# Kernel tuning notes

Measured on AMD Instinct MI355X. Metric: run time of the kernel, lower is better.

The kernel has to match this reference:

```python
import jax, jax.numpy as jnp
import numpy as np

MAX_WAVELENGTH = 1000.0

def _sine_pos(n, d):
    # keras_nlp SinePositionEncoding with max_wavelength=1000
    pos = jnp.arange(n, dtype=jnp.float32)
    i = jnp.arange(d)
    timescales = (1.0 / MAX_WAVELENGTH) ** ((2 * (i // 2)).astype(jnp.float32) / d)
    ang = pos[:, None] * timescales[None, :]  # (n, d)
    return jnp.where(i % 2 == 0, jnp.sin(ang), jnp.cos(ang))


def setup_inputs() -> dict:
    key = jax.random.key(0)
    ks = jax.random.split(key, 6)
    B, N, D, H, O = 4, 2048, 512, 8, 64
    inputs = jax.random.normal(ks[0], (B, N, D), jnp.float32)
    mem = jax.random.normal(ks[1], (B, H, O, O), jnp.float32) * 0.02
    # z accumulates sums of (elu(k)+1) > 0, so keep it positive
    z = jax.random.uniform(ks[2], (B, H, O), jnp.float32) + 1.0
    attn_kernel = jax.random.normal(ks[3], (D, H, O, 3), jnp.float32) * (1.0 / np.sqrt(D))
    out_kernel = jax.random.normal(ks[4], (O, H, O), jnp.float32) * (1.0 / np.sqrt(O * H))
    beta = jnp.zeros((1,), jnp.float32)
    return dict(inputs=inputs, mem=mem, z=z, attn_kernel=attn_kernel,
                out_kernel=out_kernel, beta=beta)


def reference(inputs, mem, z, attn_kernel, out_kernel, beta):
    B, N, D = inputs.shape
    x = inputs + _sine_pos(N, D)[None].astype(inputs.dtype)
    # fused QKV projection: (B,N,H,dims,3)
    kvq = jnp.einsum('bni,ihok->bnhok', x, attn_kernel)
    k, v, q = kvq[..., 0], kvq[..., 1], kvq[..., 2]
    # linear-attention memory readout
    q_elu = jax.nn.elu(q) + 1.0
    num = jnp.einsum('bhdo,bnhd->bnho', mem, q_elu)
    den = jnp.einsum('bhd,bnhd->bnh', z, q_elu)[..., None] + 1e-8
    A_mem = num / den
    # delta-rule state update
    k_elu = jax.nn.elu(k) + 1.0
    next_mem = mem + jnp.einsum('bnhz,bnho->bhzo', k_elu, v - A_mem)
    next_z = z + k_elu.sum(axis=1)
    # causal softmax attention over the chunk
    scale = jnp.sqrt(jnp.asarray(D, inputs.dtype))
    qk = jnp.einsum('bnho,bkho->bhnk', q, k) / scale
    mask = -(1.0 - jnp.tril(jnp.ones((N, N), inputs.dtype))) * 1e10
    A_soft = jax.nn.softmax(qk + mask, axis=-1)
    A_dot = jnp.einsum('bhnk,bkho->bnho', A_soft, v)
    # sigmoid-gated mix + output projection
    g = jax.nn.sigmoid(beta)  # (1,) broadcasts
    A = g * A_mem + (1.0 - g) * A_dot
    out = jnp.einsum('bnhi,iho->bno', A, out_kernel)
    return out, next_mem, next_z
```

## Files before the change

### kernel.cpp

```cpp
#include <hip/hip_runtime.h>
#include <hip/hip_bf16.h>
#include <math.h>

#define BB 4
#define SEQ 2048
#define DIM 512
#define NH 8
#define HD 64

typedef __attribute__((ext_vector_type(8))) short short8;
typedef __attribute__((ext_vector_type(4))) float f32x4;

static __device__ inline ushort f2bf(float f) {
    __hip_bfloat16 h = __float2bfloat16(f);
    union { __hip_bfloat16 h; ushort u; } cv;
    cv.h = h;
    return cv.u;
}
static __device__ inline float bf2f(ushort u) {
    return __uint_as_float((uint)u << 16);
}

#define GLOAD16(g, l)                                                          \
    __builtin_amdgcn_global_load_lds(                                          \
        (const __attribute__((address_space(1))) uint32_t*)(g),                \
        (__attribute__((address_space(3))) uint32_t*)(l), 16, 0, 0)

__global__ __launch_bounds__(256) void pos_add_bf16_kernel(const float* __restrict__ in,
                                                           ushort* __restrict__ xbf) {
    int idx = blockIdx.x * 256 + threadIdx.x;
    int p = idx & 255;
    int n = (idx >> 8) & 2047;
    float e = (float)(2 * p) * (1.0f / 512.0f);
    float ts = __expf(-6.907755278982137f * e);
    float arev = (float)n * (ts * 0.15915494309189535f);
    float f = arev - floorf(arev);
    float s = __builtin_amdgcn_sinf(f);
    float c = __builtin_amdgcn_cosf(f);
    float2 v = *(const float2*)(in + (size_t)idx * 2);
    uint pack = (uint)f2bf(v.x + s) | ((uint)f2bf(v.y + c) << 16);
    ((uint*)xbf)[idx] = pack;
}

__global__ __launch_bounds__(256) void wconv_kernel(const float* __restrict__ w,
                                                    ushort* __restrict__ wt) {
    __shared__ float tile[64][129];
    int ib = blockIdx.x;
    int jb = blockIdx.y;
    int t = threadIdx.x;
    #pragma unroll
    for (int u = 0; u < 8; ++u) {
        int idx = u * 1024 + t * 4;
        int r = idx >> 7, j = idx & 127;
        float4 v = *(const float4*)(w + (size_t)(ib * 64 + r) * 1536 + jb * 128 + j);
        tile[r][j] = v.x; tile[r][j + 1] = v.y; tile[r][j + 2] = v.z; tile[r][j + 3] = v.w;
    }
    __syncthreads();
    int j = t >> 1;
    int rh = (t & 1) * 32;
    int jg = jb * 128 + j;
    int h = jg / 192;
    int rem = jg - h * 192;
    int o = rem / 3;
    int c = rem - o * 3;
    int nrow = c * 512 + h * 64 + o;
    #pragma unroll
    for (int s8 = 0; s8 < 4; ++s8) {
        short8 pk;
        #pragma unroll
        for (int q = 0; q < 8; ++q) pk[q] = (short)f2bf(tile[rh + s8 * 8 + q][j]);
        *(short8*)(wt + (size_t)nrow * 512 + ib * 64 + rh + s8 * 8) = pk;
    }
}

__global__ __launch_bounds__(256) void wout_conv_kernel(const float* __restrict__ wo,
                                                        ushort* __restrict__ wobf) {
    int g = blockIdx.x * 256 + threadIdx.x;
    int o2 = g >> 9, k = g & 511;
    int h = k >> 6, i = k & 63;
    wobf[g] = f2bf(wo[(size_t)i * 512 + h * 64 + o2]);
}

__global__ __launch_bounds__(256) void qkv_mfma_kernel(const ushort* __restrict__ xbf,
                                                       const ushort* __restrict__ wt,
                                                       ushort* __restrict__ kbf,
                                                       ushort* __restrict__ vbf,
                                                       ushort* __restrict__ qbf) {
    __shared__ __align__(16) ushort As[128 * 32];
    __shared__ __align__(16) ushort Bs[128 * 32];
    int t = threadIdx.x;
    int w = t >> 6, lane = t & 63, l15 = lane & 15, lg = lane >> 4;
    int wr = w >> 1, wc = w & 1;
    int m0 = blockIdx.x * 128;
    int by = blockIdx.y;
    int n0 = by * 128;
    f32x4 acc[4][4] = {};
    int srow = t >> 2, scol = (t & 3) * 8;
    const ushort* ag = xbf + (size_t)(m0 + srow) * 512 + scol;
    const ushort* bg = wt + (size_t)(n0 + srow) * 512 + scol;
    ushort* as_dst = As + t * 8;
    ushort* bs_dst = Bs + t * 8;

    for (int k0 = 0; k0 < 512; k0 += 32) {
        __syncthreads();
        GLOAD16(ag + k0, as_dst);
        GLOAD16(ag + k0 + 64 * 512, as_dst + 64 * 32);
        GLOAD16(bg + k0, bs_dst);
        GLOAD16(bg + k0 + 64 * 512, bs_dst + 64 * 32);
        __syncthreads();
        short8 af[4], bf[4];
        #pragma unroll
        for (int mi = 0; mi < 4; ++mi)
            af[mi] = *(const short8*)&As[(wr * 64 + mi * 16 + l15) * 32 + lg * 8];
        #pragma unroll
        for (int ni = 0; ni < 4; ++ni)
            bf[ni] = *(const short8*)&Bs[(wc * 64 + ni * 16 + l15) * 32 + lg * 8];
        #pragma unroll
        for (int mi = 0; mi < 4; ++mi)
            #pragma unroll
            for (int ni = 0; ni < 4; ++ni)
                acc[mi][ni] = __builtin_amdgcn_mfma_f32_16x16x32_bf16(af[mi], bf[ni], acc[mi][ni], 0, 0, 0);
    }

    ushort* dst = (by < 4) ? kbf : (by < 8) ? vbf : qbf;
    int ho0 = (by & 3) * 128 + wc * 64;
    int mb = m0 + wr * 64;
    #pragma unroll
    for (int mi = 0; mi < 4; ++mi)
        #pragma unroll
        for (int ni = 0; ni < 4; ++ni)
            #pragma unroll
            for (int r = 0; r < 4; ++r)
                dst[(size_t)(mb + mi * 16 + lg * 4 + r) * 512 + ho0 + ni * 16 + l15] =
                    f2bf(acc[mi][ni][r]);
}

__global__ __launch_bounds__(256) void vt_kernel(const ushort* __restrict__ vbf,
                                                 ushort* __restrict__ vtbf) {
    int bid = blockIdx.x;
    int nt = bid & 31;
    int bh = bid >> 5;
    int b = bh >> 3, h = bh & 7;
    __shared__ ushort tile[64][72];
    int t = threadIdx.x;
    {
        int n = t >> 2, dc = (t & 3) * 16;
        const ushort* src = vbf + (size_t)(b * 2048 + nt * 64 + n) * 512 + h * 64 + dc;
        *(short8*)&tile[n][dc] = *(const short8*)src;
        *(short8*)&tile[n][dc + 8] = *(const short8*)(src + 8);
    }
    __syncthreads();
    {
        int d = t >> 2, nc = (t & 3) * 16;
        ushort* dst = vtbf + (size_t)bh * 64 * 2048 + (size_t)d * 2048 + nt * 64 + nc;
        short8 a, bq;
        #pragma unroll
        for (int j = 0; j < 8; ++j) { a[j] = (short)tile[nc + j][d]; bq[j] = (short)tile[nc + 8 + j][d]; }
        *(short8*)dst = a;
        *(short8*)(dst + 8) = bq;
    }
}

__global__ __launch_bounds__(256) void amem_kernel(const ushort* __restrict__ qbf,
                                                   const float* __restrict__ mem,
                                                   const float* __restrict__ zin,
                                                   ushort* __restrict__ ambf) {
    int bid = blockIdx.x;
    int ntile = bid & 7;
    int h = (bid >> 3) & 7;
    int b = bid >> 6;
    __shared__ __align__(16) float mem_s[4096];
    __shared__ float z_s[64];
    int t = threadIdx.x;
    const float* msrc = mem + (size_t)(b * 8 + h) * 4096;
    #pragma unroll
    for (int u = 0; u < 16; ++u) mem_s[t + 256 * u] = msrc[t + 256 * u];
    if (t < 64) z_s[t] = zin[(b * 8 + h) * 64 + t];
    __syncthreads();
    int n = ntile * 256 + t;
    const ushort* qrow = qbf + (size_t)(b * 2048 + n) * 512 + h * 64;
    float qe[64];
    #pragma unroll
    for (int d8 = 0; d8 < 8; ++d8) {
        short8 v8 = *(const short8*)(qrow + d8 * 8);
        #pragma unroll
        for (int j = 0; j < 8; ++j) {
            float f = bf2f((ushort)v8[j]);
            qe[d8 * 8 + j] = f > 0.f ? f + 1.f : __expf(f);
        }
    }
    float den = 0.f;
    #pragma unroll
    for (int d = 0; d < 64; ++d) den += z_s[d] * qe[d];
    den += 1e-8f;
    float num[64];
    #pragma unroll
    for (int o = 0; o < 64; ++o) num[o] = 0.f;
    #pragma unroll
    for (int d = 0; d < 64; ++d) {
        float qd = qe[d];
        #pragma unroll
        for (int o4 = 0; o4 < 64; o4 += 4) {
            float4 mv = *(const float4*)&mem_s[d * 64 + o4];
            num[o4 + 0] += mv.x * qd;
            num[o4 + 1] += mv.y * qd;
            num[o4 + 2] += mv.z * qd;
            num[o4 + 3] += mv.w * qd;
        }
    }
    float inv = 1.f / den;
    ushort* dst = ambf + (size_t)(b * 2048 + n) * 512 + h * 64;
    #pragma unroll
    for (int o8 = 0; o8 < 8; ++o8) {
        short8 pk;
        #pragma unroll
        for (int j = 0; j < 8; ++j) pk[j] = (short)f2bf(num[o8 * 8 + j] * inv);
        *(short8*)(dst + o8 * 8) = pk;
    }
}

__global__ __launch_bounds__(256) void delta_part_kernel(const ushort* __restrict__ kbf,
                                                         const ushort* __restrict__ vbf,
                                                         const ushort* __restrict__ ambf,
                                                         float* __restrict__ part,
                                                         float* __restrict__ zpart) {
    int bid = blockIdx.x;
    int bh = bid & 31;
    int chunk = bid >> 5;
    int h = bh & 7, b = bh >> 3;
    __shared__ __align__(16) float ke_s[2048];
    __shared__ __align__(16) float vm_s[2048];
    int t = threadIdx.x;
    int tx = t & 15, ty = t >> 4;
    float acc[4][4] = {};
    float nz = 0.f;
    int nbase = chunk * 256;
    for (int n0 = 0; n0 < 256; n0 += 32) {
        {
            int nn = t >> 3, cc = (t & 7) * 8;
            size_t g = (size_t)(b * 2048 + nbase + n0 + nn) * 512 + h * 64 + cc;
            short8 k8 = *(const short8*)(kbf + g);
            short8 v8 = *(const short8*)(vbf + g);
            short8 a8 = *(const short8*)(ambf + g);
            #pragma unroll
            for (int j = 0; j < 8; ++j) {
                float kv = bf2f((ushort)k8[j]);
                ke_s[t * 8 + j] = kv > 0.f ? kv + 1.f : __expf(kv);
                vm_s[t * 8 + j] = bf2f((ushort)v8[j]) - bf2f((ushort)a8[j]);
            }
        }
        __syncthreads();
        #pragma unroll
        for (int nn = 0; nn < 32; ++nn) {
            float4 ka4 = *(const float4*)&ke_s[nn * 64 + ty * 4];
            float4 vv4 = *(const float4*)&vm_s[nn * 64 + tx * 4];
            float ka[4] = {ka4.x, ka4.y, ka4.z, ka4.w};
            float vv[4] = {vv4.x, vv4.y, vv4.z, vv4.w};
            #pragma unroll
            for (int i = 0; i < 4; ++i)
                #pragma unroll
                for (int j = 0; j < 4; ++j) acc[i][j] += ka[i] * vv[j];
        }
        if (t < 64) {
            #pragma unroll
            for (int nn = 0; nn < 32; ++nn) nz += ke_s[nn * 64 + t];
        }
        __syncthreads();
    }
    float* pdst = part + (size_t)bid * 4096;
    #pragma unroll
    for (int i = 0; i < 4; ++i)
        #pragma unroll
        for (int j = 0; j < 4; ++j)
            pdst[(ty * 4 + i) * 64 + tx * 4 + j] = acc[i][j];
    if (t < 64) zpart[bid * 64 + t] = nz;
}

__global__ __launch_bounds__(256) void delta_reduce_kernel(const float* __restrict__ part,
                                                           const float* __restrict__ zpart,
                                                           const float* __restrict__ mem,
                                                           const float* __restrict__ zin,
                                                           float* __restrict__ out_mem,
                                                           float* __restrict__ out_z) {
    int bh = blockIdx.x;
    int t = threadIdx.x;
    #pragma unroll
    for (int q = 0; q < 4; ++q) {
        int e = t * 16 + q * 4;
        float4 acc = *(const float4*)(mem + (size_t)bh * 4096 + e);
        #pragma unroll
        for (int c = 0; c < 8; ++c) {
            float4 pv = *(const float4*)(part + (size_t)(c * 32 + bh) * 4096 + e);
            acc.x += pv.x; acc.y += pv.y; acc.z += pv.z; acc.w += pv.w;
        }
        *(float4*)(out_mem + (size_t)bh * 4096 + e) = acc;
    }
    if (t < 64) {
        float z = zin[bh * 64 + t];
        #pragma unroll
        for (int c = 0; c < 8; ++c) z += zpart[(c * 32 + bh) * 64 + t];
        out_z[bh * 64 + t] = z;
    }
}

#define FL_PSTR 72
__global__ __launch_bounds__(256, 2) void flash3_kernel(const ushort* __restrict__ qbf,
                                                        const ushort* __restrict__ kbf,
                                                        const ushort* __restrict__ vtbf,
                                                        ushort* __restrict__ adbf) {
    int bid0 = blockIdx.x;
    int bid = (bid0 & 7) * 64 + (bid0 >> 3);
    int i = bid & 15;
    int h = (bid >> 4) & 7;
    int b = bid >> 7;
    __shared__ __align__(16) ushort k_s[2][4096];
    __shared__ __align__(16) ushort vt_s[2][4096];
    __shared__ __align__(16) ushort p_s[4][16 * FL_PSTR];
    int t = threadIdx.x;
    int w = t >> 6, lane = t & 63, l15 = lane & 15, lg = lane >> 4;
    const int rA = i, rB = 31 - i;
    const int sw = l15 & 7;

    const ushort* qbase = qbf + (size_t)(b * 2048) * 512 + h * 64 + lg * 8;
    short8 qfA[2], qfB[2];
    #pragma unroll
    for (int c = 0; c < 2; ++c) {
        qfA[c] = *(const short8*)(qbase + (size_t)(rA * 64 + w * 16 + l15) * 512 + c * 32);
        qfB[c] = *(const short8*)(qbase + (size_t)(rB * 64 + w * 16 + l15) * 512 + c * 32);
    }
    f32x4 oA[4] = {}, oB[4] = {};
    float mA[4], lA[4], mB[4], lB[4];
    #pragma unroll
    for (int r = 0; r < 4; ++r) { mA[r] = mB[r] = -1e30f; lA[r] = lB[r] = 0.f; }
    const float C = 0.06375875f;

    int ch0 = t, ch1 = t + 256;
    int row0 = ch0 >> 3, sc0 = (ch0 & 7) ^ (row0 & 7);
    int row1 = ch1 >> 3, sc1 = (ch1 & 7) ^ (row1 & 7);
    const ushort* kbase = kbf + (size_t)(b * 2048) * 512 + h * 64;
    const ushort* vtbase = vtbf + (size_t)(b * 8 + h) * 64 * 2048;
    ushort* pw = &p_s[w][0];

    short8 ones;
    #pragma unroll
    for (int j = 0; j < 8; ++j) ones[j] = (short)0x3F80;

    short8 kf[4][2], vf[4][2];

    auto STAGE = [&](int buf, int kt) {
        GLOAD16(kbase + (size_t)(kt * 64 + row0) * 512 + sc0 * 8, &k_s[buf][ch0 * 8]);
        GLOAD16(kbase + (size_t)(kt * 64 + row1) * 512 + sc1 * 8, &k_s[buf][ch1 * 8]);
        GLOAD16(vtbase + (size_t)row0 * 2048 + kt * 64 + sc0 * 8, &vt_s[buf][ch0 * 8]);
        GLOAD16(vtbase + (size_t)row1 * 2048 + kt * 64 + sc1 * 8, &vt_s[buf][ch1 * 8]);
    };

    auto proc = [&](const short8* qf, f32x4* oo, float* mm, float* ll, int rt, int kt) {
        f32x4 s[4];
        #pragma unroll
        for (int t4 = 0; t4 < 4; ++t4) {
            f32x4 z = {0.f, 0.f, 0.f, 0.f};
            z = __builtin_amdgcn_mfma_f32_16x16x32_bf16(qf[0], kf[t4][0], z, 0, 0, 0);
            z = __builtin_amdgcn_mfma_f32_16x16x32_bf16(qf[1], kf[t4][1], z, 0, 0, 0);
            s[t4] = z;
        }
        if (kt == rt) {
            #pragma unroll
            for (int t4 = 0; t4 < 4; ++t4) {
                int colb = t4 * 16 + l15;
                int rowb = w * 16 + lg * 4;
                #pragma unroll
                for (int r = 0; r < 4; ++r)
                    if (colb > rowb + r) s[t4][r] = -1e30f;
            }
        }
        float mt[4];
        #pragma unroll
        for (int r = 0; r < 4; ++r)
            mt[r] = fmaxf(fmaxf(s[0][r], s[1][r]), fmaxf(s[2][r], s[3][r]));
        #pragma unroll
        for (int msk = 1; msk < 16; msk <<= 1)
            #pragma unroll
            for (int r = 0; r < 4; ++r) mt[r] = fmaxf(mt[r], __shfl_xor(mt[r], msk));
        float gm = fmaxf(fmaxf(mt[0] - mm[0], mt[1] - mm[1]),
                         fmaxf(mt[2] - mm[2], mt[3] - mm[3]));
        if (__ballot(gm > 32.0f) != 0ull) {
            float corr[4];
            #pragma unroll
            for (int r = 0; r < 4; ++r) {
                float mnew = fmaxf(mm[r], mt[r]);
                corr[r] = __builtin_amdgcn_exp2f((mm[r] - mnew) * C);
                mm[r] = mnew;
            }
            #pragma unroll
            for (int dt = 0; dt < 4; ++dt)
                #pragma unroll
                for (int r = 0; r < 4; ++r) oo[dt][r] *= corr[r];
            #pragma unroll
            for (int r = 0; r < 4; ++r) ll[r] *= corr[r];
        }
        float mc[4];
        #pragma unroll
        for (int r = 0; r < 4; ++r) mc[r] = mm[r] * C;
        #pragma unroll
        for (int t4 = 0; t4 < 4; ++t4)
            #pragma unroll
            for (int r = 0; r < 4; ++r) {
                float pv = __builtin_amdgcn_exp2f(s[t4][r] * C - mc[r]);
                pw[(lg * 4 + r) * FL_PSTR + t4 * 16 + l15] = f2bf(pv);
            }
        short8 pf0 = *(const short8*)&pw[l15 * FL_PSTR + lg * 8];
        short8 pf1 = *(const short8*)&pw[l15 * FL_PSTR + 32 + lg * 8];
        f32x4 zsum = {0.f, 0.f, 0.f, 0.f};
        zsum = __builtin_amdgcn_mfma_f32_16x16x32_bf16(pf0, ones, zsum, 0, 0, 0);
        zsum = __builtin_amdgcn_mfma_f32_16x16x32_bf16(pf1, ones, zsum, 0, 0, 0);
        #pragma unroll
        for (int r = 0; r < 4; ++r) ll[r] += zsum[r];
        #pragma unroll
        for (int dt = 0; dt < 4; ++dt) {
            oo[dt] = __builtin_amdgcn_mfma_f32_16x16x32_bf16(pf0, vf[dt][0], oo[dt], 0, 0, 0);
            oo[dt] = __builtin_amdgcn_mfma_f32_16x16x32_bf16(pf1, vf[dt][1], oo[dt], 0, 0, 0);
        }
    };

    STAGE(0, 0);
    for (int kt = 0; kt <= rB; ++kt) {
        int cur = kt & 1;
        __builtin_amdgcn_s_barrier();
        if (kt < rB) {
            STAGE(cur ^ 1, kt + 1);
            asm volatile("s_waitcnt vmcnt(4)" ::: "memory");
        } else {
            asm volatile("s_waitcnt vmcnt(0)" ::: "memory");
        }
        __builtin_amdgcn_s_barrier();
        #pragma unroll
        for (int t4 = 0; t4 < 4; ++t4) {
            const ushort* kr = &k_s[cur][(t4 * 16 + l15) * 64];
            kf[t4][0] = *(const short8*)&kr[(lg ^ sw) * 8];
            kf[t4][1] = *(const short8*)&kr[((4 + lg) ^ sw) * 8];
            const ushort* vr = &vt_s[cur][(t4 * 16 + l15) * 64];
            vf[t4][0] = *(const short8*)&vr[(lg ^ sw) * 8];
            vf[t4][1] = *(const short8*)&vr[((4 + lg) ^ sw) * 8];
        }
        proc(qfB, oB, mB, lB, rB, kt);
        if (kt <= rA) proc(qfA, oA, mA, lA, rA, kt);
    }

    auto fin = [&](f32x4* oo, float* ll, int rt) {
        #pragma unroll
        for (int r = 0; r < 4; ++r) {
            float inv = 1.f / ll[r];
            ushort* dst = adbf + (size_t)(b * 2048 + rt * 64 + w * 16 + lg * 4 + r) * 512 + h * 64;
            #pragma unroll
            for (int dt = 0; dt < 4; ++dt)
                dst[dt * 16 + l15] = f2bf(oo[dt][r] * inv);
        }
    };
    fin(oA, lA, rA);
    fin(oB, lB, rB);
}

__global__ __launch_bounds__(256) void outproj_mfma_kernel(const ushort* __restrict__ ambf,
                                                           const ushort* __restrict__ adbf,
                                                           const ushort* __restrict__ wobf,
                                                           const float* __restrict__ beta,
                                                           float* __restrict__ out) {
    __shared__ __align__(16) ushort W_s[64 * 512];
    __shared__ __align__(16) ushort A_s[64 * 64];
    int t = threadIdx.x;
    int w = t >> 6, lane = t & 63, l15 = lane & 15, lg = lane >> 4;
    int m0 = blockIdx.x * 64;
    float g = 1.f / (1.f + __expf(-beta[0]));
    float gi = 1.f - g;

    #pragma unroll
    for (int p = 0; p < 16; ++p) {
        int ch = p * 256 + t;
        int row = ch >> 6, c = ch & 63;
        int cs = c ^ (row & 7);
        GLOAD16(wobf + (size_t)row * 512 + cs * 8, W_s + ch * 8);
    }

    int ar = t >> 2, ac0 = (t & 3) * 2;
    int rx = l15 & 7;
    f32x4 acc[4] = {};

    for (int ks = 0; ks < 8; ++ks) {
        size_t gofs = (size_t)(m0 + ar) * 512 + ks * 64 + ac0 * 8;
        short8 a8 = *(const short8*)(ambf + gofs);
        short8 d8 = *(const short8*)(adbf + gofs);
        short8 a9 = *(const short8*)(ambf + gofs + 8);
        short8 d9 = *(const short8*)(adbf + gofs + 8);
        short8 x0, x1;
        #pragma unroll
        for (int j = 0; j < 8; ++j) {
            x0[j] = (short)f2bf(g * bf2f((ushort)a8[j]) + gi * bf2f((ushort)d8[j]));
            x1[j] = (short)f2bf(g * bf2f((ushort)a9[j]) + gi * bf2f((ushort)d9[j]));
        }
        if (ks) __syncthreads();
        *(short8*)&A_s[(ar * 8 + (ac0 ^ (ar & 7))) * 8] = x0;
        *(short8*)&A_s[(ar * 8 + ((ac0 + 1) ^ (ar & 7))) * 8] = x1;
        __syncthreads();

        const ushort* arow = &A_s[(w * 16 + l15) * 64];
        short8 af0 = *(const short8*)&arow[(lg ^ rx) * 8];
        short8 af1 = *(const short8*)&arow[((4 + lg) ^ rx) * 8];
        #pragma unroll
        for (int ni = 0; ni < 4; ++ni) {
            const ushort* wrow = &W_s[(ni * 16 + l15) * 512];
            short8 bf0 = *(const short8*)&wrow[(ks * 8 + (lg ^ rx)) * 8];
            short8 bf1 = *(const short8*)&wrow[(ks * 8 + ((4 + lg) ^ rx)) * 8];
            acc[ni] = __builtin_amdgcn_mfma_f32_16x16x32_bf16(af0, bf0, acc[ni], 0, 0, 0);
            acc[ni] = __builtin_amdgcn_mfma_f32_16x16x32_bf16(af1, bf1, acc[ni], 0, 0, 0);
        }
    }

    #pragma unroll
    for (int ni = 0; ni < 4; ++ni)
        #pragma unroll
        for (int r = 0; r < 4; ++r)
            out[(size_t)(m0 + w * 16 + lg * 4 + r) * 64 + ni * 16 + l15] = acc[ni][r];
}

extern "C" void kernel_launch(void* const* d_in, const int* in_sizes, int n_in,
                              void* d_out, int out_size, void* d_ws, size_t ws_size,
                              hipStream_t stream) {
    const float* inputs = (const float*)d_in[0];
    const float* mem    = (const float*)d_in[1];
    const float* zin    = (const float*)d_in[2];
    const float* attnk  = (const float*)d_in[3];
    const float* outk   = (const float*)d_in[4];
    const float* beta   = (const float*)d_in[5];
    float* out = (float*)d_out;
    float* ws  = (float*)d_ws;

    ushort* am_bf = (ushort*)ws;
    ushort* ad_bf = (ushort*)(ws + 2097152);
    ushort* kbf   = (ushort*)(ws + 4194304);
    ushort* vbf   = (ushort*)(ws + 6291456);
    ushort* qbf   = (ushort*)(ws + 8388608);
    ushort* vtbf  = (ushort*)(ws + 10485760);
    ushort* xbf   = (ushort*)(ws + 12582912);
    ushort* wtbf  = (ushort*)(ws + 14680064);
    ushort* wobf  = (ushort*)(ws + 15073280);
    float*  part  = ws + 15089664;
    float*  zpart = ws + 16138240;

    float* out_main = out;
    float* out_mem  = out + 524288;
    float* out_z    = out + 655360;

    pos_add_bf16_kernel<<<8192, 256, 0, stream>>>(inputs, xbf);
    wconv_kernel<<<dim3(8, 12), 256, 0, stream>>>(attnk, wtbf);
    wout_conv_kernel<<<128, 256, 0, stream>>>(outk, wobf);
    qkv_mfma_kernel<<<dim3(64, 12), 256, 0, stream>>>(xbf, wtbf, kbf, vbf, qbf);
    vt_kernel<<<1024, 256, 0, stream>>>(vbf, vtbf);
    amem_kernel<<<256, 256, 0, stream>>>(qbf, mem, zin, am_bf);
    delta_part_kernel<<<256, 256, 0, stream>>>(kbf, vbf, am_bf, part, zpart);
    delta_reduce_kernel<<<32, 256, 0, stream>>>(part, zpart, mem, zin, out_mem, out_z);
    flash3_kernel<<<512, 256, 0, stream>>>(qbf, kbf, vtbf, ad_bf);
    outproj_mfma_kernel<<<128, 256, 0, stream>>>(am_bf, ad_bf, wobf, beta, out_main);
}
```

Baseline: 213.9 us.

## Compute linear-attention memory readout with bf16 MFMA including denominator column

Replaces the scalar per-row FMA loop of the memory readout with bf16 MFMA tiles. The memory matrix and z vector are converted to bf16 into a swizzled LDS tile, and z is appended as an extra output column so the denominator comes out of the same matrix multiply. The goal is to cut the heavy scalar FMA work and register pressure of the amem stage. In exchange mem and z are rounded to bf16, which loosens precision, and the output stores become scattered 2-byte writes.

```diff
diff --git a/kernel.cpp b/kernel.cpp
--- a/kernel.cpp
+++ b/kernel.cpp
@@ -161,61 +161,80 @@
     }
 }
 
-__global__ __launch_bounds__(256) void amem_kernel(const ushort* __restrict__ qbf,
-                                                   const float* __restrict__ mem,
-                                                   const float* __restrict__ zin,
-                                                   ushort* __restrict__ ambf) {
+__global__ __launch_bounds__(256) void amem_mfma_kernel(const ushort* __restrict__ qbf,
+                                                        const float* __restrict__ mem,
+                                                        const float* __restrict__ zin,
+                                                        ushort* __restrict__ ambf) {
     int bid = blockIdx.x;
-    int ntile = bid & 7;
+    int nt = bid & 7;
     int h = (bid >> 3) & 7;
     int b = bid >> 6;
-    __shared__ __align__(16) float mem_s[4096];
-    __shared__ float z_s[64];
-    int t = threadIdx.x;
-    const float* msrc = mem + (size_t)(b * 8 + h) * 4096;
-    #pragma unroll
-    for (int u = 0; u < 16; ++u) mem_s[t + 256 * u] = msrc[t + 256 * u];
-    if (t < 64) z_s[t] = zin[(b * 8 + h) * 64 + t];
+    __shared__ __align__(16) ushort bt_s[80 * 64];
+    int t = threadIdx.x;
+    int w = t >> 6, lane = t & 63, l15 = lane & 15, lg = lane >> 4;
+
+    {
+        int d = t >> 2;
+        int o0 = (t & 3) * 16;
+        const float* msrc = mem + (size_t)(b * 8 + h) * 4096 + (size_t)d * 64 + o0;
+        #pragma unroll
+        for (int j = 0; j < 16; ++j) {
+            int o = o0 + j;
+            int c = (d >> 3) ^ (o & 7);
+            bt_s[(o * 8 + c) * 8 + (d & 7)] = f2bf(msrc[j]);
+        }
+        if (t < 64) {
+            bt_s[(64 * 8 + (t >> 3)) * 8 + (t & 7)] = f2bf(zin[(b * 8 + h) * 64 + t]);
+        }
+    }
     __syncthreads();
-    int n = ntile * 256 + t;
-    const ushort* qrow = qbf + (size_t)(b * 2048 + n) * 512 + h * 64;
-    float qe[64];
-    #pragma unroll
-    for (int d8 = 0; d8 < 8; ++d8) {
-        short8 v8 = *(const short8*)(qrow + d8 * 8);
+
+    int sw = l15 & 7;
+    short8 bfr[5][2];
+    #pragma unroll
+    for (int n = 0; n < 5; ++n) {
+        const ushort* br = &bt_s[(n * 16 + l15) * 64];
+        bfr[n][0] = *(const short8*)&br[(lg ^ sw) * 8];
+        bfr[n][1] = *(const short8*)&br[((4 + lg) ^ sw) * 8];
+    }
+
+    int rowbase = b * 2048 + nt * 256 + w * 64;
+    f32x4 acc[4][5] = {};
+    #pragma unroll
+    for (int m = 0; m < 4; ++m) {
+        const ushort* qrow = qbf + (size_t)(rowbase + m * 16 + l15) * 512 + h * 64;
+        short8 q0 = *(const short8*)(qrow + lg * 8);
+        short8 q1 = *(const short8*)(qrow + 32 + lg * 8);
+        short8 a0, a1;
         #pragma unroll
         for (int j = 0; j < 8; ++j) {
-            float f = bf2f((ushort)v8[j]);
-            qe[d8 * 8 + j] = f > 0.f ? f + 1.f : __expf(f);
-        }
-    }
-    float den = 0.f;
-    #pragma unroll
-    for (int d = 0; d < 64; ++d) den += z_s[d] * qe[d];
-    den += 1e-8f;
-    float num[64];
-    #pragma unroll
-    for (int o = 0; o < 64; ++o) num[o] = 0.f;
-    #pragma unroll
-    for (int d = 0; d < 64; ++d) {
-        float qd = qe[d];
-        #pragma unroll
-        for (int o4 = 0; o4 < 64; o4 += 4) {
-            float4 mv = *(const float4*)&mem_s[d * 64 + o4];
-            num[o4 + 0] += mv.x * qd;
-            num[o4 + 1] += mv.y * qd;
-            num[o4 + 2] += mv.z * qd;
-            num[o4 + 3] += mv.w * qd;
-        }
-    }
-    float inv = 1.f / den;
-    ushort* dst = ambf + (size_t)(b * 2048 + n) * 512 + h * 64;
-    #pragma unroll
-    for (int o8 = 0; o8 < 8; ++o8) {
-        short8 pk;
-        #pragma unroll
-        for (int j = 0; j < 8; ++j) pk[j] = (short)f2bf(num[o8 * 8 + j] * inv);
-        *(short8*)(dst + o8 * 8) = pk;
+            float f0 = bf2f((ushort)q0[j]);
+            float f1 = bf2f((ushort)q1[j]);
+            a0[j] = (short)f2bf(f0 > 0.f ? f0 + 1.f : __expf(f0));
+            a1[j] = (short)f2bf(f1 > 0.f ? f1 + 1.f : __expf(f1));
+        }
+        #pragma unroll
+        for (int n = 0; n < 5; ++n) {
+            acc[m][n] = __builtin_amdgcn_mfma_f32_16x16x32_bf16(a0, bfr[n][0], acc[m][n], 0, 0, 0);
+            acc[m][n] = __builtin_amdgcn_mfma_f32_16x16x32_bf16(a1, bfr[n][1], acc[m][n], 0, 0, 0);
+        }
+    }
+
+    #pragma unroll
+    for (int m = 0; m < 4; ++m) {
+        float inv[4];
+        #pragma unroll
+        for (int r = 0; r < 4; ++r) {
+            float d = __shfl(acc[m][4][r], (lane & 48));
+            inv[r] = 1.f / (d + 1e-8f);
+        }
+        #pragma unroll
+        for (int r = 0; r < 4; ++r) {
+            ushort* dst = ambf + (size_t)(rowbase + m * 16 + lg * 4 + r) * 512 + h * 64;
+            #pragma unroll
+            for (int n = 0; n < 4; ++n)
+                dst[n * 16 + l15] = f2bf(acc[m][n][r] * inv[r]);
+        }
     }
 }
 
@@ -555,7 +574,7 @@
     wout_conv_kernel<<<128, 256, 0, stream>>>(outk, wobf);
     qkv_mfma_kernel<<<dim3(64, 12), 256, 0, stream>>>(xbf, wtbf, kbf, vbf, qbf);
     vt_kernel<<<1024, 256, 0, stream>>>(vbf, vtbf);
-    amem_kernel<<<256, 256, 0, stream>>>(qbf, mem, zin, am_bf);
+    amem_mfma_kernel<<<256, 256, 0, stream>>>(qbf, mem, zin, am_bf);
     delta_part_kernel<<<256, 256, 0, stream>>>(kbf, vbf, am_bf, part, zpart);
     delta_reduce_kernel<<<32, 256, 0, stream>>>(part, zpart, mem, zin, out_mem, out_z);
     flash3_kernel<<<512, 256, 0, stream>>>(qbf, kbf, vtbf, ad_bf);
```

After: 196.9 us. 1.09x faster.
